# Performance work log

Measured on AMD Instinct MI355X. Metric: run time of the kernel, lower is better.

The kernel has to match this reference:

```python
import jax, jax.numpy as jnp
import numpy as np

N, E, D = 50000, 800000, 128      # nodes, edges, input feature dim
H, HEADS, C = 128, 8, 64          # hidden units, attention heads, classes
HEAD_DIM = H // HEADS
NEG_SLOPE = 0.2


def segment_softmax(scores, seg, num_segments):
    # scores: [E, heads]; softmax over edges sharing the same destination node
    m = jax.ops.segment_max(scores, seg, num_segments=num_segments)
    ex = jnp.exp(scores - m[seg])
    s = jax.ops.segment_sum(ex, seg, num_segments=num_segments)
    return ex / (s[seg] + 1e-9)


def gcn_layer(x, src, dst, W, b):
    # mean-aggregate neighbor features along edges, then linear transform
    agg = jax.ops.segment_sum(x[src], dst, num_segments=N)          # [N, d]
    deg = jax.ops.segment_sum(jnp.ones((E,), x.dtype), dst, num_segments=N)
    agg = agg / jnp.maximum(deg, 1.0)[:, None]
    return agg @ W + b


def gat_layer(x, src, dst, Wg, a_src, a_dst, bg):
    h = (x @ Wg).reshape(N, HEADS, HEAD_DIM)                        # [N, heads, hd]
    e_s = jnp.einsum('nhd,hd->nh', h, a_src)                        # [N, heads]
    e_d = jnp.einsum('nhd,hd->nh', h, a_dst)
    scores = jax.nn.leaky_relu(e_s[src] + e_d[dst], NEG_SLOPE)      # [E, heads]
    alpha = segment_softmax(scores, dst, N)                         # [E, heads]
    msg = h[src] * alpha[:, :, None]                                # [E, heads, hd]
    out = jax.ops.segment_sum(msg, dst, num_segments=N).reshape(N, H)
    return out + bg


def setup_inputs() -> dict:
    key = jax.random.key(0)
    ks = jax.random.split(key, 12)
    s = lambda fan: 1.0 / np.sqrt(fan)
    return {
        'node_features': jax.random.normal(ks[0], (N, D), jnp.float32),
        'edge_index': jax.random.randint(ks[1], (2, E), 0, N, jnp.int32),
        'W1': jax.random.normal(ks[2], (D, H), jnp.float32) * s(D),
        'b1': jnp.zeros((H,), jnp.float32),
        'W2': jax.random.normal(ks[3], (H, H), jnp.float32) * s(H),
        'b2': jnp.zeros((H,), jnp.float32),
        'Wg': jax.random.normal(ks[4], (D, H), jnp.float32) * s(D),
        'bg': jnp.zeros((H,), jnp.float32),
        'a_src': jax.random.normal(ks[5], (HEADS, HEAD_DIM), jnp.float32) * s(HEAD_DIM),
        'a_dst': jax.random.normal(ks[6], (HEADS, HEAD_DIM), jnp.float32) * s(HEAD_DIM),
        'Wcls': jax.random.normal(ks[7], (H, C), jnp.float32) * s(H),
        'bcls': jnp.zeros((C,), jnp.float32),
        'Wl': jax.random.normal(ks[8], (H, 1), jnp.float32) * s(H),
        'bl': jnp.zeros((1,), jnp.float32),
    }


def reference(node_features, edge_index, W1, b1, W2, b2, Wg, bg, a_src, a_dst, Wcls, bcls, Wl, bl):
    src, dst = edge_index[0], edge_index[1]
    x = jax.nn.relu(gcn_layer(node_features, src, dst, W1, b1))
    x = jax.nn.relu(gcn_layer(x, src, dst, W2, b2))
    node_classification_output = jax.nn.softmax(x @ Wcls + bcls, axis=-1)  # [N, C]
    x_gat = jax.nn.relu(gat_layer(node_features, src, dst, Wg, a_src, a_dst, bg))
    link_prediction_output = jax.nn.sigmoid(x_gat @ Wl + bl)               # [N, 1]
    return (node_classification_output, link_prediction_output)
```

## Files before the change

kernel.cpp:

```cpp
#include <hip/hip_runtime.h>
#include <math.h>

#define DIM      128
#define HEADS    8
#define NCLS     64
#define NEG_SLOPE 0.2f
#define NPB32    32
#define NPB64    64
#define APAD     132
#define CAP      48

typedef unsigned int uint32;

__device__ __forceinline__ uint32 pack_bf162(float a, float b) {
    uint32 ua = __float_as_uint(a); ua += 0x7fffu + ((ua >> 16) & 1u);
    uint32 ub = __float_as_uint(b); ub += 0x7fffu + ((ub >> 16) & 1u);
    return (ua >> 16) | (ub & 0xffff0000u);
}
__device__ __forceinline__ float2 unpack_bf162(uint32 u) {
    return make_float2(__uint_as_float(u << 16), __uint_as_float(u & 0xffff0000u));
}

__global__ void fill_ell(const int* __restrict__ src, const int* __restrict__ dst,
                         int* __restrict__ cursor, int* __restrict__ ell, int E) {
    int e = blockIdx.x * blockDim.x + threadIdx.x;
    if (e >= E) return;
    int d = dst[e];
    int pos = atomicAdd(&cursor[d], 1);
    if (pos < CAP) ell[(size_t)d * CAP + pos] = src[e];
}

__global__ __launch_bounds__(256, 4)
void proj1(const float* __restrict__ x, const float* __restrict__ W1,
           const float* __restrict__ Wg, const float* __restrict__ a_src,
           const float* __restrict__ a_dst, uint32* __restrict__ zb,
           float* __restrict__ e_s, float* __restrict__ e_d, int N) {
    __shared__ float A[NPB64 * APAD];
    int n0 = blockIdx.x * NPB64;
    int tid = threadIdx.x;
    for (int idx = tid; idx < NPB64 * 32; idx += 256) {
        int nl = idx >> 5, q = idx & 31;
        int n = n0 + nl;
        float4 v = (n < N) ? ((const float4*)x)[(size_t)n * 32 + q]
                           : make_float4(0.f, 0.f, 0.f, 0.f);
        *(float4*)&A[nl * APAD + q * 4] = v;
    }
    __syncthreads();

    int fg = tid & 31, ng = tid >> 5;
    int nb = ng * 8;
    bool isG = fg >= 16;
    const float* W = isG ? (Wg + (size_t)(fg - 16) * 8) : (W1 + (size_t)fg * 8);
    float acc[8][8];
#pragma unroll
    for (int r = 0; r < 8; ++r)
#pragma unroll
        for (int c = 0; c < 8; ++c) acc[r][c] = 0.f;

#pragma unroll 4
    for (int k = 0; k < DIM; ++k) {
        float wv[8];
        *(float4*)&wv[0] = *(const float4*)(W + (size_t)k * DIM);
        *(float4*)&wv[4] = *(const float4*)(W + (size_t)k * DIM + 4);
#pragma unroll
        for (int r = 0; r < 8; ++r) {
            float a = A[(nb + r) * APAD + k];
#pragma unroll
            for (int c = 0; c < 8; ++c) acc[r][c] = fmaf(a, wv[c], acc[r][c]);
        }
    }
#pragma unroll
    for (int r = 0; r < 8; ++r) {
        int n = n0 + nb + r;
        if (n < N) {
            uint32 o[4];
#pragma unroll
            for (int c = 0; c < 4; ++c) o[c] = pack_bf162(acc[r][2 * c], acc[r][2 * c + 1]);
            *(uint4*)(zb + (size_t)n * 128 + fg * 4) = *(uint4*)o;
        }
    }
    if (isG) {
        int head = (fg - 16) >> 1, sub = ((fg - 16) & 1) * 8;
        float as[8], ad[8];
#pragma unroll
        for (int j = 0; j < 8; ++j) {
            as[j] = a_src[head * 16 + sub + j];
            ad[j] = a_dst[head * 16 + sub + j];
        }
#pragma unroll
        for (int r = 0; r < 8; ++r) {
            int n = n0 + nb + r;
            float ps = 0.f, pd = 0.f;
#pragma unroll
            for (int c = 0; c < 8; ++c) {
                ps = fmaf(acc[r][c], as[c], ps);
                pd = fmaf(acc[r][c], ad[c], pd);
            }
            ps += __shfl_xor(ps, 1);
            pd += __shfl_xor(pd, 1);
            if (n < N && !(fg & 1)) {
                e_s[n * HEADS + head] = ps;
                e_d[n * HEADS + head] = pd;
            }
        }
    }
}

__global__ __launch_bounds__(256, 8)
void mega1(const uint32* __restrict__ zb, const int* __restrict__ cursor,
           const int* __restrict__ ell, const float* __restrict__ e_s,
           const float* __restrict__ e_d, const float* __restrict__ b1,
           const float* __restrict__ bg, const float* __restrict__ Wl,
           const float* __restrict__ bl, uint32* __restrict__ x1b,
           float* __restrict__ out_link, int N) {
    int wave = threadIdx.x >> 6, lane = threadIdx.x & 63;
    int n = blockIdx.x * 4 + wave;
    if (n >= N) return;
    int eoff = lane >> 5, q = lane & 31;
    bool isH = q >= 16;
    int head = (max(q, 16) - 16) >> 1;
    float edl = e_d[n * HEADS + head];
    const uint4* zrow = (const uint4*)zb;
    size_t base = (size_t)n * CAP;
    int len = min(cursor[n], CAP);
    float acc[8];
#pragma unroll
    for (int j = 0; j < 8; ++j) acc[j] = 0.f;
    float den = 0.f;
    int it = 0;
    for (; it + 8 <= len; it += 8) {
        int s[4];
#pragma unroll
        for (int k = 0; k < 4; ++k) s[k] = ell[base + it + 2 * k + eoff];
        float es[4]; uint4 u[4];
#pragma unroll
        for (int k = 0; k < 4; ++k) {
            es[k] = e_s[s[k] * HEADS + head];
            u[k]  = zrow[(size_t)s[k] * 32 + q];
        }
#pragma unroll
        for (int k = 0; k < 4; ++k) {
            float sc = es[k] + edl;
            sc = (sc > 0.f) ? sc : NEG_SLOPE * sc;
            float ex = __expf(sc);
            den += ex;
            float w = isH ? ex : 1.f;
            float2 v0 = unpack_bf162(u[k].x), v1 = unpack_bf162(u[k].y);
            float2 v2 = unpack_bf162(u[k].z), v3 = unpack_bf162(u[k].w);
            acc[0] = fmaf(v0.x, w, acc[0]); acc[1] = fmaf(v0.y, w, acc[1]);
            acc[2] = fmaf(v1.x, w, acc[2]); acc[3] = fmaf(v1.y, w, acc[3]);
            acc[4] = fmaf(v2.x, w, acc[4]); acc[5] = fmaf(v2.y, w, acc[5]);
            acc[6] = fmaf(v3.x, w, acc[6]); acc[7] = fmaf(v3.y, w, acc[7]);
        }
    }
    for (; it < len; it += 2) {
        int e = it + eoff;
        bool valid = e < len;
        int s = ell[base + (valid ? e : it)];
        float sc = e_s[s * HEADS + head] + edl;
        sc = (sc > 0.f) ? sc : NEG_SLOPE * sc;
        float ex = __expf(sc);
        uint4 u = zrow[(size_t)s * 32 + q];
        den += valid ? ex : 0.f;
        float w = valid ? (isH ? ex : 1.f) : 0.f;
        float2 v0 = unpack_bf162(u.x), v1 = unpack_bf162(u.y);
        float2 v2 = unpack_bf162(u.z), v3 = unpack_bf162(u.w);
        acc[0] = fmaf(v0.x, w, acc[0]); acc[1] = fmaf(v0.y, w, acc[1]);
        acc[2] = fmaf(v1.x, w, acc[2]); acc[3] = fmaf(v1.y, w, acc[3]);
        acc[4] = fmaf(v2.x, w, acc[4]); acc[5] = fmaf(v2.y, w, acc[5]);
        acc[6] = fmaf(v3.x, w, acc[6]); acc[7] = fmaf(v3.y, w, acc[7]);
    }
#pragma unroll
    for (int j = 0; j < 8; ++j) acc[j] += __shfl_xor(acc[j], 32);
    den += __shfl_xor(den, 32);

    if (!isH && eoff == 0) {
        float inv = 1.f / fmaxf((float)len, 1.f);
        float4 ba = ((const float4*)b1)[2 * q];
        float4 bb = ((const float4*)b1)[2 * q + 1];
        uint4 o;
        o.x = pack_bf162(fmaxf(acc[0] * inv + ba.x, 0.f), fmaxf(acc[1] * inv + ba.y, 0.f));
        o.y = pack_bf162(fmaxf(acc[2] * inv + ba.z, 0.f), fmaxf(acc[3] * inv + ba.w, 0.f));
        o.z = pack_bf162(fmaxf(acc[4] * inv + bb.x, 0.f), fmaxf(acc[5] * inv + bb.y, 0.f));
        o.w = pack_bf162(fmaxf(acc[6] * inv + bb.z, 0.f), fmaxf(acc[7] * inv + bb.w, 0.f));
        ((uint4*)(x1b + (size_t)n * 64))[q] = o;
    }
    float p = 0.f;
    if (isH && eoff == 0) {
        float inva = 1.f / (den + 1e-9f);
        int hq = q - 16;
        float4 ga = ((const float4*)bg)[2 * hq];
        float4 gb = ((const float4*)bg)[2 * hq + 1];
        float4 wa = ((const float4*)Wl)[2 * hq];
        float4 wb = ((const float4*)Wl)[2 * hq + 1];
        p = fmaf(fmaxf(acc[0] * inva + ga.x, 0.f), wa.x, p);
        p = fmaf(fmaxf(acc[1] * inva + ga.y, 0.f), wa.y, p);
        p = fmaf(fmaxf(acc[2] * inva + ga.z, 0.f), wa.z, p);
        p = fmaf(fmaxf(acc[3] * inva + ga.w, 0.f), wa.w, p);
        p = fmaf(fmaxf(acc[4] * inva + gb.x, 0.f), wb.x, p);
        p = fmaf(fmaxf(acc[5] * inva + gb.y, 0.f), wb.y, p);
        p = fmaf(fmaxf(acc[6] * inva + gb.z, 0.f), wb.z, p);
        p = fmaf(fmaxf(acc[7] * inva + gb.w, 0.f), wb.w, p);
    }
#pragma unroll
    for (int off = 1; off < 64; off <<= 1) p += __shfl_xor(p, off);
    if (lane == 0) out_link[n] = 1.f / (1.f + expf(-(p + bl[0])));
}

__global__ __launch_bounds__(256, 4)
void proj2(const uint32* __restrict__ x1b, const float* __restrict__ W2,
           uint32* __restrict__ y2b, int N) {
    __shared__ float A[NPB64 * APAD];
    int n0 = blockIdx.x * NPB64;
    int tid = threadIdx.x;
    for (int idx = tid; idx < NPB64 * 64; idx += 256) {
        int nl = idx >> 6, q = idx & 63;
        int n = n0 + nl;
        float2 v = (n < N) ? unpack_bf162(x1b[(size_t)n * 64 + q]) : make_float2(0.f, 0.f);
        A[nl * APAD + 2 * q]     = v.x;
        A[nl * APAD + 2 * q + 1] = v.y;
    }
    __syncthreads();
    int fg = tid & 15, ng = tid >> 4;
    int nb = ng * 4;
    float acc[4][8];
#pragma unroll
    for (int r = 0; r < 4; ++r)
#pragma unroll
        for (int c = 0; c < 8; ++c) acc[r][c] = 0.f;
    const float4* W4 = (const float4*)W2;
#pragma unroll 4
    for (int k = 0; k < DIM; ++k) {
        float wv[8];
        *(float4*)&wv[0] = W4[k * 32 + fg * 2];
        *(float4*)&wv[4] = W4[k * 32 + fg * 2 + 1];
#pragma unroll
        for (int r = 0; r < 4; ++r) {
            float a = A[(nb + r) * APAD + k];
#pragma unroll
            for (int c = 0; c < 8; ++c) acc[r][c] = fmaf(a, wv[c], acc[r][c]);
        }
    }
#pragma unroll
    for (int r = 0; r < 4; ++r) {
        int n = n0 + nb + r;
        if (n < N) {
            uint32 o[4];
#pragma unroll
            for (int c = 0; c < 4; ++c) o[c] = pack_bf162(acc[r][2 * c], acc[r][2 * c + 1]);
            *(uint4*)(y2b + (size_t)n * 64 + fg * 4) = *(uint4*)o;
        }
    }
}

__global__ __launch_bounds__(256, 8)
void mega2(const uint32* __restrict__ y2b, const int* __restrict__ cursor,
           const int* __restrict__ ell, const float* __restrict__ b2,
           const float* __restrict__ Wcls, const float* __restrict__ bcls,
           float* __restrict__ out_cls, int N) {
    __shared__ float A[NPB32 * APAD];
    int tid = threadIdx.x;
    int wave = tid >> 6, lane = tid & 63;
    int eoff = lane >> 4, q = lane & 15;
    int n0 = blockIdx.x * NPB32;
    const uint4* yrow = (const uint4*)y2b;

    for (int i = 0; i < 8; ++i) {
        int nl = wave * 8 + i;
        int n = n0 + nl;
        int len = (n < N) ? min(cursor[n], CAP) : 0;
        size_t base = (size_t)n * CAP;
        float acc[8];
#pragma unroll
        for (int j = 0; j < 8; ++j) acc[j] = 0.f;
        int it = 0;
        for (; it + 8 <= len; it += 8) {
            int s[2];
#pragma unroll
            for (int k = 0; k < 2; ++k) s[k] = ell[base + it + 4 * k + eoff];
            uint4 u[2];
#pragma unroll
            for (int k = 0; k < 2; ++k) u[k] = yrow[(size_t)s[k] * 16 + q];
#pragma unroll
            for (int k = 0; k < 2; ++k) {
                float2 v0 = unpack_bf162(u[k].x), v1 = unpack_bf162(u[k].y);
                float2 v2 = unpack_bf162(u[k].z), v3 = unpack_bf162(u[k].w);
                acc[0] += v0.x; acc[1] += v0.y; acc[2] += v1.x; acc[3] += v1.y;
                acc[4] += v2.x; acc[5] += v2.y; acc[6] += v3.x; acc[7] += v3.y;
            }
        }
        for (; it < len; it += 4) {
            int e = it + eoff;
            bool valid = e < len;
            int s = ell[base + (valid ? e : it)];
            uint4 u = yrow[(size_t)s * 16 + q];
            float w = valid ? 1.f : 0.f;
            float2 v0 = unpack_bf162(u.x), v1 = unpack_bf162(u.y);
            float2 v2 = unpack_bf162(u.z), v3 = unpack_bf162(u.w);
            acc[0] = fmaf(v0.x, w, acc[0]); acc[1] = fmaf(v0.y, w, acc[1]);
            acc[2] = fmaf(v1.x, w, acc[2]); acc[3] = fmaf(v1.y, w, acc[3]);
            acc[4] = fmaf(v2.x, w, acc[4]); acc[5] = fmaf(v2.y, w, acc[5]);
            acc[6] = fmaf(v3.x, w, acc[6]); acc[7] = fmaf(v3.y, w, acc[7]);
        }
#pragma unroll
        for (int j = 0; j < 8; ++j) {
            acc[j] += __shfl_xor(acc[j], 16);
            acc[j] += __shfl_xor(acc[j], 32);
        }
        if (eoff == 0) {
            float inv = 1.f / fmaxf((float)len, 1.f);
            float4 ba = ((const float4*)b2)[2 * q];
            float4 bb = ((const float4*)b2)[2 * q + 1];
            float4 xa, xb2;
            xa.x = fmaxf(acc[0] * inv + ba.x, 0.f); xa.y = fmaxf(acc[1] * inv + ba.y, 0.f);
            xa.z = fmaxf(acc[2] * inv + ba.z, 0.f); xa.w = fmaxf(acc[3] * inv + ba.w, 0.f);
            xb2.x = fmaxf(acc[4] * inv + bb.x, 0.f); xb2.y = fmaxf(acc[5] * inv + bb.y, 0.f);
            xb2.z = fmaxf(acc[6] * inv + bb.z, 0.f); xb2.w = fmaxf(acc[7] * inv + bb.w, 0.f);
            *(float4*)&A[nl * APAD + 8 * q]     = xa;
            *(float4*)&A[nl * APAD + 8 * q + 4] = xb2;
        }
    }
    __syncthreads();

    int fg = tid & 15, ng = tid >> 4;
    int nm = ng * 2, c0 = fg * 4;
    float accC[2][4];
#pragma unroll
    for (int r = 0; r < 2; ++r)
#pragma unroll
        for (int c = 0; c < 4; ++c) accC[r][c] = 0.f;
    const float4* Wc4 = (const float4*)Wcls;
#pragma unroll 4
    for (int k = 0; k < DIM; ++k) {
        float a0 = A[nm * APAD + k];
        float a1 = A[(nm + 1) * APAD + k];
        float wv[4];
        *(float4*)&wv[0] = Wc4[k * 16 + fg];
#pragma unroll
        for (int c = 0; c < 4; ++c) {
            accC[0][c] = fmaf(a0, wv[c], accC[0][c]);
            accC[1][c] = fmaf(a1, wv[c], accC[1][c]);
        }
    }
    float4 bv = ((const float4*)bcls)[fg];
    float cb[4] = {bv.x, bv.y, bv.z, bv.w};
#pragma unroll
    for (int r = 0; r < 2; ++r) {
        int n = n0 + nm + r;
        float l[4];
        float m = -1e30f;
#pragma unroll
        for (int c = 0; c < 4; ++c) { l[c] = accC[r][c] + cb[c]; m = fmaxf(m, l[c]); }
        for (int off = 1; off < 16; off <<= 1) m = fmaxf(m, __shfl_xor(m, off));
        float s = 0.f;
#pragma unroll
        for (int c = 0; c < 4; ++c) { l[c] = expf(l[c] - m); s += l[c]; }
        for (int off = 1; off < 16; off <<= 1) s += __shfl_xor(s, off);
        float invs = 1.f / s;
        if (n < N) {
            float4 o = {l[0] * invs, l[1] * invs, l[2] * invs, l[3] * invs};
            *(float4*)(out_cls + (size_t)n * NCLS + c0) = o;
        }
    }
}

extern "C" void kernel_launch(void* const* d_in, const int* in_sizes, int n_in,
                              void* d_out, int out_size, void* d_ws, size_t ws_size,
                              hipStream_t stream) {
    const float* xin   = (const float*)d_in[0];
    const int*   eidx  = (const int*)  d_in[1];
    const float* W1    = (const float*)d_in[2];
    const float* b1    = (const float*)d_in[3];
    const float* W2    = (const float*)d_in[4];
    const float* b2    = (const float*)d_in[5];
    const float* Wg    = (const float*)d_in[6];
    const float* bg    = (const float*)d_in[7];
    const float* a_src = (const float*)d_in[8];
    const float* a_dst = (const float*)d_in[9];
    const float* Wcls  = (const float*)d_in[10];
    const float* bcls  = (const float*)d_in[11];
    const float* Wl    = (const float*)d_in[12];
    const float* bl    = (const float*)d_in[13];

    const int N = in_sizes[0] / DIM;
    const int E = in_sizes[1] / 2;
    const int* src = eidx;
    const int* dst = eidx + E;

    int*    cursor = (int*)d_ws;
    int*    ell    = cursor + ((N + 4) & ~3);
    float*  e_s    = (float*)(ell + (size_t)N * CAP);
    float*  e_d    = e_s + (size_t)N * HEADS;
    uint32* zb     = (uint32*)(e_d + (size_t)N * HEADS);
    uint32* x1b    = zb + (size_t)N * 128;
    uint32* y2b    = zb;

    float* out_cls  = (float*)d_out;
    float* out_link = out_cls + (size_t)N * NCLS;

    int blkE   = (E + 255) / 256;
    int blkN4  = (N + 3) / 4;
    int blkN32 = (N + NPB32 - 1) / NPB32;
    int blkN64 = (N + NPB64 - 1) / NPB64;

    hipMemsetAsync(cursor, 0, (size_t)N * sizeof(int), stream);
    fill_ell<<<blkE, 256, 0, stream>>>(src, dst, cursor, ell, E);

    proj1<<<blkN64, 256, 0, stream>>>(xin, W1, Wg, a_src, a_dst, zb, e_s, e_d, N);

    mega1<<<blkN4, 256, 0, stream>>>(zb, cursor, ell, e_s, e_d,
                                     b1, bg, Wl, bl, x1b, out_link, N);

    proj2<<<blkN64, 256, 0, stream>>>(x1b, W2, y2b, N);

    mega2<<<blkN32, 256, 0, stream>>>(y2b, cursor, ell, b2,
                                      Wcls, bcls, out_cls, N);
}
```

Baseline: 369.3 us.

## Fuse second GCN projection into aggregation kernel, aggregating before transform

Removes the separate proj2 kernel and instead has mega2 gather and mean-aggregate the bf16 layer-1 activations directly. It then applies the W2 matmul, bias and ReLU in shared memory before the classifier matmul. This uses linearity (mean then matmul equals matmul then mean) to skip writing and re-reading the projected y2 buffer and one kernel launch. In exchange mega2 carries an extra 128x128 matmul per block and another barrier round, which may lower occupancy under the 8-block launch bound.

```diff
diff --git a/kernel.cpp b/kernel.cpp
--- a/kernel.cpp
+++ b/kernel.cpp
@@ -207,63 +207,17 @@
     if (lane == 0) out_link[n] = 1.f / (1.f + expf(-(p + bl[0])));
 }
 
-__global__ __launch_bounds__(256, 4)
-void proj2(const uint32* __restrict__ x1b, const float* __restrict__ W2,
-           uint32* __restrict__ y2b, int N) {
-    __shared__ float A[NPB64 * APAD];
-    int n0 = blockIdx.x * NPB64;
-    int tid = threadIdx.x;
-    for (int idx = tid; idx < NPB64 * 64; idx += 256) {
-        int nl = idx >> 6, q = idx & 63;
-        int n = n0 + nl;
-        float2 v = (n < N) ? unpack_bf162(x1b[(size_t)n * 64 + q]) : make_float2(0.f, 0.f);
-        A[nl * APAD + 2 * q]     = v.x;
-        A[nl * APAD + 2 * q + 1] = v.y;
-    }
-    __syncthreads();
-    int fg = tid & 15, ng = tid >> 4;
-    int nb = ng * 4;
-    float acc[4][8];
-#pragma unroll
-    for (int r = 0; r < 4; ++r)
-#pragma unroll
-        for (int c = 0; c < 8; ++c) acc[r][c] = 0.f;
-    const float4* W4 = (const float4*)W2;
-#pragma unroll 4
-    for (int k = 0; k < DIM; ++k) {
-        float wv[8];
-        *(float4*)&wv[0] = W4[k * 32 + fg * 2];
-        *(float4*)&wv[4] = W4[k * 32 + fg * 2 + 1];
-#pragma unroll
-        for (int r = 0; r < 4; ++r) {
-            float a = A[(nb + r) * APAD + k];
-#pragma unroll
-            for (int c = 0; c < 8; ++c) acc[r][c] = fmaf(a, wv[c], acc[r][c]);
-        }
-    }
-#pragma unroll
-    for (int r = 0; r < 4; ++r) {
-        int n = n0 + nb + r;
-        if (n < N) {
-            uint32 o[4];
-#pragma unroll
-            for (int c = 0; c < 4; ++c) o[c] = pack_bf162(acc[r][2 * c], acc[r][2 * c + 1]);
-            *(uint4*)(y2b + (size_t)n * 64 + fg * 4) = *(uint4*)o;
-        }
-    }
-}
-
 __global__ __launch_bounds__(256, 8)
-void mega2(const uint32* __restrict__ y2b, const int* __restrict__ cursor,
-           const int* __restrict__ ell, const float* __restrict__ b2,
-           const float* __restrict__ Wcls, const float* __restrict__ bcls,
-           float* __restrict__ out_cls, int N) {
+void mega2(const uint32* __restrict__ x1b, const int* __restrict__ cursor,
+           const int* __restrict__ ell, const float* __restrict__ W2,
+           const float* __restrict__ b2, const float* __restrict__ Wcls,
+           const float* __restrict__ bcls, float* __restrict__ out_cls, int N) {
     __shared__ float A[NPB32 * APAD];
     int tid = threadIdx.x;
     int wave = tid >> 6, lane = tid & 63;
     int eoff = lane >> 4, q = lane & 15;
     int n0 = blockIdx.x * NPB32;
-    const uint4* yrow = (const uint4*)y2b;
+    const uint4* yrow = (const uint4*)x1b;
 
     for (int i = 0; i < 8; ++i) {
         int nl = wave * 8 + i;
@@ -309,21 +263,53 @@
         }
         if (eoff == 0) {
             float inv = 1.f / fmaxf((float)len, 1.f);
-            float4 ba = ((const float4*)b2)[2 * q];
-            float4 bb = ((const float4*)b2)[2 * q + 1];
-            float4 xa, xb2;
-            xa.x = fmaxf(acc[0] * inv + ba.x, 0.f); xa.y = fmaxf(acc[1] * inv + ba.y, 0.f);
-            xa.z = fmaxf(acc[2] * inv + ba.z, 0.f); xa.w = fmaxf(acc[3] * inv + ba.w, 0.f);
-            xb2.x = fmaxf(acc[4] * inv + bb.x, 0.f); xb2.y = fmaxf(acc[5] * inv + bb.y, 0.f);
-            xb2.z = fmaxf(acc[6] * inv + bb.z, 0.f); xb2.w = fmaxf(acc[7] * inv + bb.w, 0.f);
+            float4 xa, xb;
+            xa.x = acc[0] * inv; xa.y = acc[1] * inv; xa.z = acc[2] * inv; xa.w = acc[3] * inv;
+            xb.x = acc[4] * inv; xb.y = acc[5] * inv; xb.z = acc[6] * inv; xb.w = acc[7] * inv;
             *(float4*)&A[nl * APAD + 8 * q]     = xa;
-            *(float4*)&A[nl * APAD + 8 * q + 4] = xb2;
+            *(float4*)&A[nl * APAD + 8 * q + 4] = xb;
         }
     }
     __syncthreads();
 
     int fg = tid & 15, ng = tid >> 4;
-    int nm = ng * 2, c0 = fg * 4;
+    int f0 = fg * 8, nm = ng * 2;
+    float acc2[2][8];
+#pragma unroll
+    for (int r = 0; r < 2; ++r)
+#pragma unroll
+        for (int c = 0; c < 8; ++c) acc2[r][c] = 0.f;
+    const float4* W4 = (const float4*)W2;
+#pragma unroll 4
+    for (int k = 0; k < DIM; ++k) {
+        float a0 = A[nm * APAD + k];
+        float a1 = A[(nm + 1) * APAD + k];
+        float wv[8];
+        *(float4*)&wv[0] = W4[k * 32 + fg * 2];
+        *(float4*)&wv[4] = W4[k * 32 + fg * 2 + 1];
+#pragma unroll
+        for (int c = 0; c < 8; ++c) {
+            acc2[0][c] = fmaf(a0, wv[c], acc2[0][c]);
+            acc2[1][c] = fmaf(a1, wv[c], acc2[1][c]);
+        }
+    }
+    float bias[8];
+    *(float4*)&bias[0] = ((const float4*)b2)[fg * 2];
+    *(float4*)&bias[4] = ((const float4*)b2)[fg * 2 + 1];
+#pragma unroll
+    for (int r = 0; r < 2; ++r)
+#pragma unroll
+        for (int c = 0; c < 8; ++c)
+            acc2[r][c] = fmaxf(acc2[r][c] + bias[c], 0.f);
+    __syncthreads();
+#pragma unroll
+    for (int r = 0; r < 2; ++r) {
+        *(float4*)&A[(nm + r) * APAD + f0]     = *(float4*)&acc2[r][0];
+        *(float4*)&A[(nm + r) * APAD + f0 + 4] = *(float4*)&acc2[r][4];
+    }
+    __syncthreads();
+
+    int c0 = fg * 4;
     float accC[2][4];
 #pragma unroll
     for (int r = 0; r < 2; ++r)
@@ -393,7 +379,6 @@
     float*  e_d    = e_s + (size_t)N * HEADS;
     uint32* zb     = (uint32*)(e_d + (size_t)N * HEADS);
     uint32* x1b    = zb + (size_t)N * 128;
-    uint32* y2b    = zb;
 
     float* out_cls  = (float*)d_out;
     float* out_link = out_cls + (size_t)N * NCLS;
@@ -411,8 +396,6 @@
     mega1<<<blkN4, 256, 0, stream>>>(zb, cursor, ell, e_s, e_d,
                                      b1, bg, Wl, bl, x1b, out_link, N);
 
-    proj2<<<blkN64, 256, 0, stream>>>(x1b, W2, y2b, N);
-
-    mega2<<<blkN32, 256, 0, stream>>>(y2b, cursor, ell, b2,
+    mega2<<<blkN32, 256, 0, stream>>>(x1b, cursor, ell, W2, b2,
                                       Wcls, bcls, out_cls, N);
 }
```

New measurement: 385.7 us. 4.4% more time.
